# Kernel tuning notes

Hardware: AMD Instinct MI355X
Metric: run time of the kernel (lower is better)

Reference implementation:

```python
import jax, jax.numpy as jnp
import numpy as np

BASE_SIGMAS = (2.0, 4.0, 8.0, 16.0, 32.0)
REF_LEN = 512
TRUNCATE = 4.0
STAT_WIN = 16
TEMP = 0.7
EPS = 1e-6


def _gauss_kernels(T):
    """Centered normalized Gaussian kernels, sigmas scaled by T/REF_LEN (numpy, static)."""
    s = T / REF_LEN
    ks = []
    for b in BASE_SIGMAS:
        sig = round(b * s, 4)
        R = min(max(1, int(TRUNCATE * sig + 0.5)), max(1, (T - 1) // 2))
        n = np.arange(-R, R + 1, dtype=np.float32)
        k = np.exp(-0.5 * (n / max(sig, 1e-6)) ** 2)
        ks.append((k / (k.sum() + 1e-12)).astype(np.float32))
    return ks


def _corr1d(x_pad, k):
    """Depthwise cross-correlation along time. x_pad:[B,Tp,C], k:[K] -> [B,Tp-K+1,C].
    Same kernel for every channel: fold C into batch."""
    B, Tp, C = x_pad.shape
    K = k.shape[0]
    xc = jnp.moveaxis(x_pad, 1, 2).reshape(B * C, 1, Tp)
    kern = jnp.asarray(k, x_pad.dtype).reshape(1, 1, K)
    y = jax.lax.conv_general_dilated(xc, kern, (1,), 'VALID')  # [B*C,1,Tout]
    Tout = Tp - K + 1
    return jnp.moveaxis(y.reshape(B, C, Tout), 1, 2)


def _pad_reflect_t(x, lp, rp):
    return jnp.pad(x, ((0, 0), (lp, rp), (0, 0)), mode='reflect')


def reference(x, W1, b1, W2, b2, W3, b3):
    B, T, C = x.shape
    # 1) multi-scale depthwise Gaussian smoothing -> Y [B,T,C,K]
    Ys = []
    for k in _gauss_kernels(T):
        pad = k.shape[0] // 2
        Ys.append(_corr1d(_pad_reflect_t(x, pad, pad), k))
    Y = jnp.stack(Ys, axis=-1)

    # 2) windowed local statistics via correlation kernels (== torch unfold + reduce)
    win = max(2, min(STAT_WIN, T))
    lp, rp = (win - 1) // 2, win // 2
    xp = _pad_reflect_t(x, lp, rp)
    mean_k = np.full((win,), 1.0 / win, dtype=np.float32)
    t = np.arange(win, dtype=np.float32)
    t_c = t - t.mean()
    t_var = float((t_c ** 2).sum())
    mean = _corr1d(xp, mean_k)                           # [B,T,C]
    ex2 = _corr1d(xp * xp, mean_k)
    var = jnp.maximum(ex2 - mean * mean, 0.0)
    cov = _corr1d(xp, t_c)                               # sum(x * t_centered) over window
    slope = cov / (t_var + EPS)

    std = jnp.sqrt(var + EPS)
    z = jnp.clip((x - mean) / std, -10.0, 10.0)
    log_var = jnp.log(var + EPS) / 10.0
    norm_slope = jnp.clip(slope / (std + EPS), -10.0, 10.0)
    feats = jnp.stack([z, log_var, norm_slope], axis=-1)  # [B,T,C,3]

    # 3) conditioning MLP (Linear/GELU/Linear/GELU/Linear), exact-erf GELU like torch
    h = jax.nn.gelu(jnp.einsum('btcf,hf->btch', feats, W1) + b1, approximate=False)
    h = jax.nn.gelu(jnp.einsum('btch,gh->btcg', h, W2) + b2, approximate=False)
    logits = jnp.einsum('btcg,kg->btck', h, W3) + b3      # [B,T,C,K]
    w = jax.nn.softmax(logits / TEMP, axis=-1)

    # 4) gated combine
    return (Y * w).sum(axis=-1)


def setup_inputs() -> dict:
    key = jax.random.key(0)
    ks = jax.random.split(key, 7)
    B, T, C, H, K = 32, 2048, 64, 32, 5
    return {
        'x': jax.random.normal(ks[0], (B, T, C), dtype=jnp.float32),
        'W1': jax.random.normal(ks[1], (H, 3), dtype=jnp.float32) * 0.3,
        'b1': jax.random.normal(ks[2], (H,), dtype=jnp.float32) * 0.1,
        'W2': jax.random.normal(ks[3], (H, H), dtype=jnp.float32) * 0.15,
        'b2': jax.random.normal(ks[4], (H,), dtype=jnp.float32) * 0.1,
        'W3': jax.random.normal(ks[5], (K, H), dtype=jnp.float32) * 0.05,
        'b3': jnp.zeros((K,), dtype=jnp.float32),
    }
```

## Files before the change

### kernel.cpp

```cpp
#include <hip/hip_runtime.h>
#include <hip/hip_fp16.h>
#include <math.h>

#define TT 2048
#define CC 64
#define BB 32
#define PAD 512
#define ROWL 3136

typedef __attribute__((ext_vector_type(8))) short short8;
typedef __attribute__((ext_vector_type(4))) float float4v;
typedef _Float16 half8 __attribute__((ext_vector_type(8)));

#define NSTEPS 67
__device__ unsigned short g_afrag_hi[NSTEPS * 64 * 8];

__device__ __forceinline__ float fast_rcp(float x) { return __builtin_amdgcn_rcpf(x); }
__device__ __forceinline__ float fast_exp2(float x) { return __builtin_amdgcn_exp2f(x); }
__device__ __forceinline__ float fast_log2(float x) { return __builtin_amdgcn_logf(x); }

__device__ __forceinline__ unsigned short f2bf(float x) {
  union { float f; unsigned u; } v; v.f = x;
  unsigned r = (v.u + 0x7FFFu + ((v.u >> 16) & 1u)) >> 16;
  return (unsigned short)r;
}
__device__ __forceinline__ unsigned h2u(__half2 h) { union { __half2 h; unsigned u; } c; c.h = h; return c.u; }

__device__ __forceinline__ __half2 gelu_h2(__half2 x) {
  const __half2 c1 = __float2half2_rn(-0.10294217f);
  const __half2 c0 = __float2half2_rn(-2.3020231f);
  const __half2 one = __float2half2_rn(1.0f);
  __half2 u = __hmul2(x, x);
  __half2 w = __hmul2(x, __hfma2(c1, u, c0));
  __half2 e = h2exp2(w);
  return __hmul2(x, h2rcp(__hadd2(e, one)));
}

__device__ __forceinline__ void init_frag_body(int bid, int nb, int tid,
                                               float* ktap, double* ssum) {
  const int   Rr[5]  = {32, 64, 128, 256, 512};
  const float sg[5]  = {8.f, 16.f, 32.f, 64.f, 128.f};
  const int   off[5] = {0, 72, 208, 472, 984};

  for (int idx = tid; idx < 2016; idx += 256) {
    int s = (idx < 72) ? 0 : (idx < 208) ? 1 : (idx < 472) ? 2 : (idx < 984) ? 3 : 4;
    int d = idx - off[s];
    float v = 0.f;
    if (d <= 2 * Rr[s]) {
      float n = (float)(d - Rr[s]) / sg[s];
      v = __expf(-0.5f * n * n);
    }
    ktap[idx] = v;
  }
  __syncthreads();
  if (tid < 5) {
    double sum = 0.0;
    for (int d = 0; d <= 2 * Rr[tid]; ++d) sum += (double)ktap[off[tid] + d];
    ssum[tid] = 1.0 / (sum + 1e-12);
  }
  __syncthreads();
  for (int idx = tid; idx < 2016; idx += 256) {
    int s = (idx < 72) ? 0 : (idx < 208) ? 1 : (idx < 472) ? 2 : (idx < 984) ? 3 : 4;
    ktap[idx] *= (float)ssum[s];
  }
  __syncthreads();

  const int cum[5] = {0, 3, 8, 17, 34};
  for (int e = bid * 256 + tid; e < NSTEPS * 64; e += nb * 256) {
    int stg = e >> 6, lane = e & 63;
    int s = (stg < 3) ? 0 : (stg < 8) ? 1 : (stg < 17) ? 2 : (stg < 34) ? 3 : 4;
    int st = stg - cum[s];
    int i = lane & 15, h = lane >> 4;
    for (int e2 = 0; e2 < 8; ++e2) {
      int d = st * 32 + 8 * h + e2 - i;
      float v = (d >= 0 && d <= 2 * Rr[s]) ? ktap[off[s] + d] : 0.f;
      g_afrag_hi[e * 8 + e2] = f2bf(v);
    }
  }
}

__global__ void init_frag() {
  __shared__ float ktap[2016];
  __shared__ double ssum[5];
  init_frag_body(blockIdx.x, gridDim.x, threadIdx.x, ktap, ssum);
}

__global__ void transpose_in(const float* __restrict__ x, unsigned short* __restrict__ xT) {
  __shared__ float tile[64][65];
  __shared__ float ktap[2016];
  __shared__ double ssum[5];
  const int tid = threadIdx.x;
  const int b = blockIdx.x >> 5;
  const int t0 = (blockIdx.x & 31) * 64;

  const float* src = x + ((size_t)b * TT + t0) * CC;
  #pragma unroll
  for (int k = 0; k < 16; ++k) {
    int idx = k * 256 + tid;
    int row = idx >> 6, col = idx & 63;
    tile[row][col] = src[(size_t)row * CC + col];
  }
  __syncthreads();
  unsigned short* dst = xT + (size_t)b * CC * TT + t0;
  #pragma unroll
  for (int k = 0; k < 16; ++k) {
    int idx = k * 256 + tid;
    int c = idx >> 6, tt = idx & 63;
    dst[(size_t)c * TT + tt] = f2bf(tile[tt][c]);
  }
  if (blockIdx.x < 8) init_frag_body(blockIdx.x, 8, tid, ktap, ssum);
}

__global__ void transpose_out(const float* __restrict__ outT, float* __restrict__ out) {
  __shared__ float tile[64][65];
  const int tid = threadIdx.x;
  const int b = blockIdx.x >> 5;
  const int t0 = (blockIdx.x & 31) * 64;

  const float* src = outT + (size_t)b * CC * TT + t0;
  #pragma unroll
  for (int k = 0; k < 16; ++k) {
    int idx = k * 256 + tid;
    int cc2 = idx >> 6, tt = idx & 63;
    tile[cc2][tt] = src[(size_t)cc2 * TT + tt];
  }
  __syncthreads();
  float* dst = out + ((size_t)b * TT + t0) * CC;
  #pragma unroll
  for (int k = 0; k < 16; ++k) {
    int idx = k * 256 + tid;
    int tt = idx >> 6, cc2 = idx & 63;
    dst[(size_t)tt * CC + cc2] = tile[cc2][tt];
  }
}

template <int WSPATH>
__launch_bounds__(256, 5)
__global__ void fused_main_t(const float* __restrict__ x, const unsigned short* __restrict__ xT,
                             const float* __restrict__ W1, const float* __restrict__ b1,
                             const float* __restrict__ W2, const float* __restrict__ b2,
                             const float* __restrict__ W3, const float* __restrict__ b3,
                             float* __restrict__ outT, float* __restrict__ out) {
  __shared__ unsigned short row_hi[ROWL];
  __shared__ __half gbuf[8][5][16][18];

  const int tid = threadIdx.x;
  const int blk = blockIdx.x;
  const int c = blk & (CC - 1);
  const int b = blk >> 6;

  if (WSPATH) {
    const unsigned short* xtr = xT + (size_t)(b * CC + c) * TT;
    for (int i2 = tid; i2 < ROWL; i2 += 256) {
      int t = i2 - PAD;
      t = (t < 0) ? -t : t;
      t = (t >= TT) ? (2 * TT - 2 - t) : t;
      row_hi[i2] = xtr[t];
    }
  } else {
    const float* xrow = x + (size_t)b * TT * CC + c;
    for (int i2 = tid; i2 < ROWL; i2 += 256) {
      int t = i2 - PAD;
      t = (t < 0) ? -t : t;
      t = (t >= TT) ? (2 * TT - 2 - t) : t;
      row_hi[i2] = f2bf(xrow[(size_t)t * CC]);
    }
  }
  __syncthreads();

  const int t0 = tid * 8;
  const int lane = tid & 63;
  const int wvi = tid >> 6;

  {
    float w24[24];
    {
      const unsigned short* ph = &row_hi[PAD + t0 - 8];
      unsigned hw[12];
      *(uint4*)&hw[0] = *(const uint4*)ph;
      *(uint4*)&hw[4] = *(const uint4*)(ph + 8);
      *(uint4*)&hw[8] = *(const uint4*)(ph + 16);
      #pragma unroll
      for (int m2 = 0; m2 < 12; ++m2) {
        union { unsigned u; float f; } a, bb;
        a.u  = (hw[m2] & 0xFFFFu) << 16;
        bb.u = hw[m2] & 0xFFFF0000u;
        w24[2 * m2]     = a.f;
        w24[2 * m2 + 1] = bb.f;
      }
    }

    float sm = 0.f, sq = 0.f, scv = 0.f;
    #pragma unroll
    for (int j = 0; j < 16; ++j) {
      float v = w24[1 + j];
      sm += v;
      sq  = fmaf(v, v, sq);
      scv = fmaf(v, (float)j - 7.5f, scv);
    }

    #pragma unroll
    for (int i = 0; i < 8; ++i) {
      const float xv   = w24[i + 8];
      const float mean = sm * 0.0625f;
      const float ex2  = sq * 0.0625f;
      const float var  = fmaxf(ex2 - mean * mean, 0.f);
      const float slope = scv * (1.0f / 340.0f);
      const float stdv = sqrtf(var + 1e-6f);
      float z = (xv - mean) * fast_rcp(stdv);
      z = fminf(fmaxf(z, -10.f), 10.f);
      float lv = fast_log2(var + 1e-6f) * 0.069314718f;
      float ns = slope * fast_rcp(stdv + 1e-6f);
      ns = fminf(fmaxf(ns, -10.f), 10.f);

      const int e = t0 + i;
      const int ch = e >> 8, rr = e & 15, pp = (e >> 4) & 15;
      gbuf[ch][0][rr][pp] = __float2half(z);
      gbuf[ch][1][rr][pp] = __float2half(lv);
      gbuf[ch][2][rr][pp] = __float2half(ns);

      if (i < 7) {
        const float xo = w24[i + 1], xn = w24[i + 17];
        scv = fmaf(8.5f, xo, fmaf(7.5f, xn, scv - sm));
        sm += (xn - xo);
        sq = fmaf(xn, xn, sq);
        sq = fmaf(-xo, xo, sq);
      }
    }
  }

  {
    const int kg = lane >> 4;
    const int m  = lane & 15;
    const int ch0 = 2 * wvi, ch1 = 2 * wvi + 1;

    half8 w2f0, w2f1;
    {
      const float* p0 = W2 + (size_t)m * 32 + 8 * kg;
      const float* p1 = W2 + (size_t)(16 + m) * 32 + 8 * kg;
      #pragma unroll
      for (int e2 = 0; e2 < 8; ++e2) {
        w2f0[e2] = (_Float16)p0[e2];
        w2f1[e2] = (_Float16)p1[e2];
      }
    }
    half8 w3f;
    #pragma unroll
    for (int e2 = 0; e2 < 8; ++e2) {
      w3f[e2] = (m < 5) ? (_Float16)W3[m * 32 + 8 * kg + e2] : (_Float16)0.f;
    }

    __half2 w1z[4], w1l[4], w1n[4], b1p[4];
    #pragma unroll
    for (int p = 0; p < 4; ++p) {
      int n0 = 8 * kg + 2 * p;
      w1z[p] = __halves2half2(__float2half(W1[n0 * 3 + 0]), __float2half(W1[n0 * 3 + 3]));
      w1l[p] = __halves2half2(__float2half(W1[n0 * 3 + 1]), __float2half(W1[n0 * 3 + 4]));
      w1n[p] = __halves2half2(__float2half(W1[n0 * 3 + 2]), __float2half(W1[n0 * 3 + 5]));
      b1p[p] = __halves2half2(__float2half(b1[n0]), __float2half(b1[n0 + 1]));
    }
    float4v b2a = *(const float4v*)(b2 + 4 * kg);
    float4v b2b = *(const float4v*)(b2 + 16 + 4 * kg);
    const float b30 = b3[0], b31 = b3[1], b32 = b3[2], b33 = b3[3], b34 = b3[4];
    const float kS = 2.0609929f;

    const int srcA = (kg & 1) * 32 + m;
    const int srcB = srcA + 16;
    const bool hiHalf = (kg >= 2);

    auto do_col = [&](int ch, int pp) {
      __half2 z2 = __half2half2(gbuf[ch][0][m][pp]);
      __half2 l2 = __half2half2(gbuf[ch][1][m][pp]);
      __half2 n2 = __half2half2(gbuf[ch][2][m][pp]);

      union { __half2 h2[4]; half8 h8; } bu;
      #pragma unroll
      for (int p = 0; p < 4; ++p) {
        __half2 pre = __hfma2(w1z[p], z2, b1p[p]);
        pre = __hfma2(w1l[p], l2, pre);
        pre = __hfma2(w1n[p], n2, pre);
        bu.h2[p] = gelu_h2(pre);
      }

      float4v acc0 = {0.f,0.f,0.f,0.f}, acc1 = {0.f,0.f,0.f,0.f};
      acc0 = __builtin_amdgcn_mfma_f32_16x16x32_f16(w2f0, bu.h8, acc0, 0, 0, 0);
      acc1 = __builtin_amdgcn_mfma_f32_16x16x32_f16(w2f1, bu.h8, acc1, 0, 0, 0);

      __half2 hh0 = __floats2half2_rn(acc0[0] + b2a[0], acc0[1] + b2a[1]);
      __half2 hh1 = __floats2half2_rn(acc0[2] + b2a[2], acc0[3] + b2a[3]);
      __half2 hh2 = __floats2half2_rn(acc1[0] + b2b[0], acc1[1] + b2b[1]);
      __half2 hh3 = __floats2half2_rn(acc1[2] + b2b[2], acc1[3] + b2b[3]);
      hh0 = gelu_h2(hh0); hh1 = gelu_h2(hh1); hh2 = gelu_h2(hh2); hh3 = gelu_h2(hh3);

      unsigned XA0 = __shfl(h2u(hh0), srcA);
      unsigned XA1 = __shfl(h2u(hh1), srcA);
      unsigned XA2 = __shfl(h2u(hh2), srcA);
      unsigned XA3 = __shfl(h2u(hh3), srcA);
      unsigned XB0 = __shfl(h2u(hh0), srcB);
      unsigned XB1 = __shfl(h2u(hh1), srcB);
      unsigned XB2 = __shfl(h2u(hh2), srcB);
      unsigned XB3 = __shfl(h2u(hh3), srcB);
      union { unsigned u[4]; half8 h8; } b2f;
      b2f.u[0] = hiHalf ? XA2 : XA0;
      b2f.u[1] = hiHalf ? XA3 : XA1;
      b2f.u[2] = hiHalf ? XB2 : XB0;
      b2f.u[3] = hiHalf ? XB3 : XB1;

      float4v d2 = {0.f,0.f,0.f,0.f};
      d2 = __builtin_amdgcn_mfma_f32_16x16x32_f16(w3f, b2f.h8, d2, 0, 0, 0);

      float lg0 = __shfl(d2[0], m) + b30;
      float lg1 = __shfl(d2[1], m) + b31;
      float lg2 = __shfl(d2[2], m) + b32;
      float lg3 = __shfl(d2[3], m) + b33;
      float lg4 = __shfl(d2[0], m + 16) + b34;

      float e0 = fast_exp2(lg0 * kS);
      float e1 = fast_exp2(lg1 * kS);
      float e2 = fast_exp2(lg2 * kS);
      float e3 = fast_exp2(lg3 * kS);
      float e4 = fast_exp2(lg4 * kS);
      const float rs = fast_rcp(e0 + e1 + e2 + e3 + e4);

      float gw = e0;
      gw = (kg == 1) ? e1 : gw;
      gw = (kg == 2) ? e2 : gw;
      gw = (kg == 3) ? e3 : gw;
      gbuf[ch][kg][m][pp] = __float2half(gw * rs);
      if (kg == 0) gbuf[ch][4][m][pp] = __float2half(e4 * rs);
    };

    #pragma unroll 1
    for (int pp = 0; pp < 16; ++pp) {
      do_col(ch0, pp);
      do_col(ch1, pp);
    }
  }

  {
    const int hq = lane >> 4, p = lane & 15;
    const int ch0 = 2 * wvi, ch1 = 2 * wvi + 1;

    const int Rs[5]    = {32, 64, 128, 256, 512};
    const int steps[5] = {3, 5, 9, 17, 33};
    const int cum[5]   = {0, 3, 8, 17, 34};

    float4v o0 = {0.f,0.f,0.f,0.f}, o1 = {0.f,0.f,0.f,0.f};

    #pragma unroll 1
    for (int s = 0; s < 5; ++s) {
      float4v a0 = {0.f,0.f,0.f,0.f}, a1 = {0.f,0.f,0.f,0.f};
      const int eb0 = PAD + 256 * ch0 - Rs[s] + 16 * p + 8 * hq;
      const int eb1 = eb0 + 256;
      const unsigned short* ahb = g_afrag_hi + (size_t)cum[s] * 512 + lane * 8;

      for (int st = 0; st < steps[s]; ++st) {
        short8 kh = *(const short8*)(ahb + st * 512);
        short8 b0h = *(const short8*)(&row_hi[eb0 + st * 32]);
        short8 b1h = *(const short8*)(&row_hi[eb1 + st * 32]);
        a0 = __builtin_amdgcn_mfma_f32_16x16x32_bf16(kh, b0h, a0, 0, 0, 0);
        a1 = __builtin_amdgcn_mfma_f32_16x16x32_bf16(kh, b1h, a1, 0, 0, 0);
      }
      #pragma unroll
      for (int r = 0; r < 4; ++r) {
        o0[r] = fmaf(__half2float(gbuf[ch0][s][4 * hq + r][p]), a0[r], o0[r]);
        o1[r] = fmaf(__half2float(gbuf[ch1][s][4 * hq + r][p]), a1[r], o1[r]);
      }
    }

    if (WSPATH) {
      float* orow = outT + (size_t)(b * CC + c) * TT;
      *(float4v*)(orow + 256 * ch0 + 16 * p + 4 * hq) = o0;
      *(float4v*)(orow + 256 * ch1 + 16 * p + 4 * hq) = o1;
    } else {
      const size_t obase = (size_t)b * TT * CC + c;
      #pragma unroll
      for (int r = 0; r < 4; ++r) {
        out[obase + (size_t)(256 * ch0 + 16 * p + 4 * hq + r) * CC] = o0[r];
        out[obase + (size_t)(256 * ch1 + 16 * p + 4 * hq + r) * CC] = o1[r];
      }
    }
  }
}

extern "C" void kernel_launch(void* const* d_in, const int* in_sizes, int n_in,
                              void* d_out, int out_size, void* d_ws, size_t ws_size,
                              hipStream_t stream) {
  const float* x  = (const float*)d_in[0];
  const float* W1 = (const float*)d_in[1];
  const float* b1 = (const float*)d_in[2];
  const float* W2 = (const float*)d_in[3];
  const float* b2 = (const float*)d_in[4];
  const float* W3 = (const float*)d_in[5];
  const float* b3 = (const float*)d_in[6];
  float* outp = (float*)d_out;

  const size_t xt_bytes  = (size_t)BB * CC * TT * sizeof(unsigned short);
  const size_t ot_bytes  = (size_t)BB * CC * TT * sizeof(float);
  if (ws_size >= xt_bytes + ot_bytes) {
    unsigned short* xT = (unsigned short*)d_ws;
    float* outT = (float*)((char*)d_ws + xt_bytes);
    hipLaunchKernelGGL(transpose_in, dim3(BB * 32), dim3(256), 0, stream, x, xT);
    hipLaunchKernelGGL(fused_main_t<1>, dim3(BB * CC), dim3(256), 0, stream,
                       x, xT, W1, b1, W2, b2, W3, b3, outT, outp);
    hipLaunchKernelGGL(transpose_out, dim3(BB * 32), dim3(256), 0, stream, outT, outp);
  } else {
    hipLaunchKernelGGL(init_frag, dim3(8), dim3(256), 0, stream);
    hipLaunchKernelGGL(fused_main_t<0>, dim3(BB * CC), dim3(256), 0, stream,
                       x, (const unsigned short*)nullptr, W1, b1, W2, b2, W3, b3,
                       (float*)nullptr, outp);
  }
}
```

Baseline: 151.1 us.

## Split each channel row into two time halves per block with swizzled gate buffer

Each block now handles half of a (batch, channel) time row (1024 steps plus halo) instead of the full 2048, doubling the grid and halving per-thread work. Shared memory drops: the row buffer shrinks and the gate buffer loses its padding, using an XOR swizzle against bank conflicts. Launch bounds rise to 8 blocks per CU for more occupancy. In exchange, each block reloads the 1024-element reflect halo, so input traffic into shared memory goes up and each wave carries less independent MFMA work to hide latency.

```diff
diff --git a/kernel.cpp b/kernel.cpp
--- a/kernel.cpp
+++ b/kernel.cpp
@@ -5,8 +5,8 @@
 #define TT 2048
 #define CC 64
 #define BB 32
-#define PAD 512
-#define ROWL 3136
+#define PADL 512
+#define ROWW 2112
 
 typedef __attribute__((ext_vector_type(8))) short short8;
 typedef __attribute__((ext_vector_type(4))) float float4v;
@@ -135,32 +135,34 @@
 }
 
 template <int WSPATH>
-__launch_bounds__(256, 5)
+__launch_bounds__(256, 8)
 __global__ void fused_main_t(const float* __restrict__ x, const unsigned short* __restrict__ xT,
                              const float* __restrict__ W1, const float* __restrict__ b1,
                              const float* __restrict__ W2, const float* __restrict__ b2,
                              const float* __restrict__ W3, const float* __restrict__ b3,
                              float* __restrict__ outT, float* __restrict__ out) {
-  __shared__ unsigned short row_hi[ROWL];
-  __shared__ __half gbuf[8][5][16][18];
+  __shared__ unsigned short row_hi[ROWW];
+  __shared__ __half gbuf[4][5][16][16];
 
   const int tid = threadIdx.x;
   const int blk = blockIdx.x;
   const int c = blk & (CC - 1);
-  const int b = blk >> 6;
+  const int tblk = (blk >> 6) & 1;
+  const int b = blk >> 7;
+  const int tbase = tblk * 1024;
 
   if (WSPATH) {
     const unsigned short* xtr = xT + (size_t)(b * CC + c) * TT;
-    for (int i2 = tid; i2 < ROWL; i2 += 256) {
-      int t = i2 - PAD;
+    for (int i2 = tid; i2 < ROWW; i2 += 256) {
+      int t = tbase + i2 - PADL;
       t = (t < 0) ? -t : t;
       t = (t >= TT) ? (2 * TT - 2 - t) : t;
       row_hi[i2] = xtr[t];
     }
   } else {
     const float* xrow = x + (size_t)b * TT * CC + c;
-    for (int i2 = tid; i2 < ROWL; i2 += 256) {
-      int t = i2 - PAD;
+    for (int i2 = tid; i2 < ROWW; i2 += 256) {
+      int t = tbase + i2 - PADL;
       t = (t < 0) ? -t : t;
       t = (t >= TT) ? (2 * TT - 2 - t) : t;
       row_hi[i2] = f2bf(xrow[(size_t)t * CC]);
@@ -168,14 +170,17 @@
   }
   __syncthreads();
 
-  const int t0 = tid * 8;
   const int lane = tid & 63;
   const int wvi = tid >> 6;
 
   {
+    const int kk = tid >> 1;
+    const int sh = (tid & 1) * 4;
+    const int t0 = tid * 4;
+
     float w24[24];
     {
-      const unsigned short* ph = &row_hi[PAD + t0 - 8];
+      const unsigned short* ph = &row_hi[PADL + 8 * kk - 8];
       unsigned hw[12];
       *(uint4*)&hw[0] = *(const uint4*)ph;
       *(uint4*)&hw[4] = *(const uint4*)(ph + 8);
@@ -193,15 +198,15 @@
     float sm = 0.f, sq = 0.f, scv = 0.f;
     #pragma unroll
     for (int j = 0; j < 16; ++j) {
-      float v = w24[1 + j];
+      float v = w24[sh + 1 + j];
       sm += v;
       sq  = fmaf(v, v, sq);
       scv = fmaf(v, (float)j - 7.5f, scv);
     }
 
     #pragma unroll
-    for (int i = 0; i < 8; ++i) {
-      const float xv   = w24[i + 8];
+    for (int i = 0; i < 4; ++i) {
+      const float xv   = w24[sh + i + 8];
       const float mean = sm * 0.0625f;
       const float ex2  = sq * 0.0625f;
       const float var  = fmaxf(ex2 - mean * mean, 0.f);
@@ -215,12 +220,13 @@
 
       const int e = t0 + i;
       const int ch = e >> 8, rr = e & 15, pp = (e >> 4) & 15;
-      gbuf[ch][0][rr][pp] = __float2half(z);
-      gbuf[ch][1][rr][pp] = __float2half(lv);
-      gbuf[ch][2][rr][pp] = __float2half(ns);
-
-      if (i < 7) {
-        const float xo = w24[i + 1], xn = w24[i + 17];
+      const int ppx = pp ^ ((rr >> 2) << 2);
+      gbuf[ch][0][rr][ppx] = __float2half(z);
+      gbuf[ch][1][rr][ppx] = __float2half(lv);
+      gbuf[ch][2][rr][ppx] = __float2half(ns);
+
+      if (i < 3) {
+        const float xo = w24[sh + i + 1], xn = w24[sh + i + 17];
         scv = fmaf(8.5f, xo, fmaf(7.5f, xn, scv - sm));
         sm += (xn - xo);
         sq = fmaf(xn, xn, sq);
@@ -232,7 +238,8 @@
   {
     const int kg = lane >> 4;
     const int m  = lane & 15;
-    const int ch0 = 2 * wvi, ch1 = 2 * wvi + 1;
+    const int ch = wvi;
+    const int mx = (m >> 2) << 2;
 
     half8 w2f0, w2f1;
     {
@@ -268,10 +275,12 @@
     const int srcB = srcA + 16;
     const bool hiHalf = (kg >= 2);
 
-    auto do_col = [&](int ch, int pp) {
-      __half2 z2 = __half2half2(gbuf[ch][0][m][pp]);
-      __half2 l2 = __half2half2(gbuf[ch][1][m][pp]);
-      __half2 n2 = __half2half2(gbuf[ch][2][m][pp]);
+    #pragma unroll 1
+    for (int pp = 0; pp < 16; ++pp) {
+      const int ppx = pp ^ mx;
+      __half2 z2 = __half2half2(gbuf[ch][0][m][ppx]);
+      __half2 l2 = __half2half2(gbuf[ch][1][m][ppx]);
+      __half2 n2 = __half2half2(gbuf[ch][2][m][ppx]);
 
       union { __half2 h2[4]; half8 h8; } bu;
       #pragma unroll
@@ -326,58 +335,46 @@
       gw = (kg == 1) ? e1 : gw;
       gw = (kg == 2) ? e2 : gw;
       gw = (kg == 3) ? e3 : gw;
-      gbuf[ch][kg][m][pp] = __float2half(gw * rs);
-      if (kg == 0) gbuf[ch][4][m][pp] = __float2half(e4 * rs);
-    };
-
-    #pragma unroll 1
-    for (int pp = 0; pp < 16; ++pp) {
-      do_col(ch0, pp);
-      do_col(ch1, pp);
+      gbuf[ch][kg][m][ppx] = __float2half(gw * rs);
+      if (kg == 0) gbuf[ch][4][m][ppx] = __float2half(e4 * rs);
     }
   }
 
   {
     const int hq = lane >> 4, p = lane & 15;
-    const int ch0 = 2 * wvi, ch1 = 2 * wvi + 1;
 
     const int Rs[5]    = {32, 64, 128, 256, 512};
     const int steps[5] = {3, 5, 9, 17, 33};
     const int cum[5]   = {0, 3, 8, 17, 34};
 
-    float4v o0 = {0.f,0.f,0.f,0.f}, o1 = {0.f,0.f,0.f,0.f};
+    float4v o0 = {0.f,0.f,0.f,0.f};
 
     #pragma unroll 1
     for (int s = 0; s < 5; ++s) {
-      float4v a0 = {0.f,0.f,0.f,0.f}, a1 = {0.f,0.f,0.f,0.f};
-      const int eb0 = PAD + 256 * ch0 - Rs[s] + 16 * p + 8 * hq;
-      const int eb1 = eb0 + 256;
+      float4v a0 = {0.f,0.f,0.f,0.f};
+      const int eb0 = PADL + 256 * wvi - Rs[s] + 16 * p + 8 * hq;
       const unsigned short* ahb = g_afrag_hi + (size_t)cum[s] * 512 + lane * 8;
 
       for (int st = 0; st < steps[s]; ++st) {
         short8 kh = *(const short8*)(ahb + st * 512);
         short8 b0h = *(const short8*)(&row_hi[eb0 + st * 32]);
-        short8 b1h = *(const short8*)(&row_hi[eb1 + st * 32]);
         a0 = __builtin_amdgcn_mfma_f32_16x16x32_bf16(kh, b0h, a0, 0, 0, 0);
-        a1 = __builtin_amdgcn_mfma_f32_16x16x32_bf16(kh, b1h, a1, 0, 0, 0);
       }
       #pragma unroll
       for (int r = 0; r < 4; ++r) {
-        o0[r] = fmaf(__half2float(gbuf[ch0][s][4 * hq + r][p]), a0[r], o0[r]);
-        o1[r] = fmaf(__half2float(gbuf[ch1][s][4 * hq + r][p]), a1[r], o1[r]);
+        const int row = 4 * hq + r;
+        o0[r] = fmaf(__half2float(gbuf[wvi][s][row][p ^ (hq << 2)]), a0[r], o0[r]);
       }
     }
 
     if (WSPATH) {
       float* orow = outT + (size_t)(b * CC + c) * TT;
-      *(float4v*)(orow + 256 * ch0 + 16 * p + 4 * hq) = o0;
-      *(float4v*)(orow + 256 * ch1 + 16 * p + 4 * hq) = o1;
+      *(float4v*)(orow + tbase + 256 * wvi + 16 * p + 4 * hq) = o0;
     } else {
       const size_t obase = (size_t)b * TT * CC + c;
       #pragma unroll
       for (int r = 0; r < 4; ++r) {
-        out[obase + (size_t)(256 * ch0 + 16 * p + 4 * hq + r) * CC] = o0[r];
-        out[obase + (size_t)(256 * ch1 + 16 * p + 4 * hq + r) * CC] = o1[r];
+        out[obase + (size_t)(tbase + 256 * wvi + 16 * p + 4 * hq + r) * CC] = o0[r];
       }
     }
   }
@@ -401,12 +398,12 @@
     unsigned short* xT = (unsigned short*)d_ws;
     float* outT = (float*)((char*)d_ws + xt_bytes);
     hipLaunchKernelGGL(transpose_in, dim3(BB * 32), dim3(256), 0, stream, x, xT);
-    hipLaunchKernelGGL(fused_main_t<1>, dim3(BB * CC), dim3(256), 0, stream,
+    hipLaunchKernelGGL(fused_main_t<1>, dim3(BB * CC * 2), dim3(256), 0, stream,
                        x, xT, W1, b1, W2, b2, W3, b3, outT, outp);
     hipLaunchKernelGGL(transpose_out, dim3(BB * 32), dim3(256), 0, stream, outT, outp);
   } else {
     hipLaunchKernelGGL(init_frag, dim3(8), dim3(256), 0, stream);
-    hipLaunchKernelGGL(fused_main_t<0>, dim3(BB * CC), dim3(256), 0, stream,
+    hipLaunchKernelGGL(fused_main_t<0>, dim3(BB * CC * 2), dim3(256), 0, stream,
                        x, (const unsigned short*)nullptr, W1, b1, W2, b2, W3, b3,
                        (float*)nullptr, outp);
   }
```

After: 160.0 us. 5.9% more time.
